# Kernel optimization log

Measured on AMD Instinct MI355X. Metric: run time of the kernel, lower is better.

The kernel has to match this reference:

```python
import jax, jax.numpy as jnp
import numpy as np

KS = 16
FREQ = jnp.array([0., 1., 2., 4., 8., 16., 32., 64.], dtype=jnp.float32)  # [0]+[2^i], d=8
TWO_PI = 2.0 * np.pi


def softplus_b10(x):
    # torch F.softplus(x, beta=10, threshold=1): linear when beta*x > threshold
    bx = 10.0 * x
    return jnp.where(bx > 1.0, x, jnp.log1p(jnp.exp(jnp.minimum(bx, 1.0))) / 10.0)


def grid_sample_2d(img, gx, gy):
    # img: (C, H, W) complex; gx,gy: (N,) in [-1,1]. Bilinear, align_corners=True,
    # zero padding -- matches torch.nn.functional.grid_sample. Returns (C, N).
    C, H, W = img.shape
    ix = (gx + 1.0) * 0.5 * (W - 1)
    iy = (gy + 1.0) * 0.5 * (H - 1)
    ix0 = jnp.floor(ix)
    iy0 = jnp.floor(iy)
    wx = ix - ix0
    wy = iy - iy0

    def corner(iyc, ixc, w):
        valid = (ixc >= 0) & (ixc <= W - 1) & (iyc >= 0) & (iyc <= H - 1)
        ii = jnp.clip(ixc, 0, W - 1).astype(jnp.int32)
        jj = jnp.clip(iyc, 0, H - 1).astype(jnp.int32)
        return img[:, jj, ii] * (w * valid)[None, :]

    return (corner(iy0, ix0, (1 - wx) * (1 - wy))
            + corner(iy0, ix0 + 1, wx * (1 - wy))
            + corner(iy0 + 1, ix0, (1 - wx) * wy)
            + corner(iy0 + 1, ix0 + 1, wx * wy))


def batch_irfft(P, x):
    # P: (ks, d, N) complex; x: (N,) in [-1,1]. Trig-weighted inverse rFFT reduce.
    xx = (x + 1.0) * 0.5
    ang = TWO_PI * xx[:, None] * FREQ[None, :]            # (N, d)
    scale = jnp.where(FREQ > 0, 2.0, 1.0)
    c = jnp.cos(ang) * scale
    s = jnp.sin(ang) * scale
    return jnp.einsum('kdn,nd->kn', P.real, c) - jnp.einsum('kdn,nd->kn', P.imag, s)


def reference(xyz, bound, alpha_params, Pu_re, Pu_im, Pv_re, Pv_im, Pw_re, Pw_im):
    alpha = softplus_b10(alpha_params)[0]
    Pu = jnp.fft.ifftn((Pu_re + 1j * Pu_im) * alpha, axes=(3, 4))  # (1,ks,dx,Ny,Nz)
    Pv = jnp.fft.ifftn((Pv_re + 1j * Pv_im) * alpha, axes=(2, 4))  # (1,ks,Nx,dy,Nz)
    Pw = jnp.fft.ifftn((Pw_re + 1j * Pw_im) * alpha, axes=(2, 3))  # (1,ks,Nx,Ny,dz)

    xyzn = xyz / bound
    xs, ys, zs = xyzn[:, 0], xyzn[:, 1], xyzn[:, 2]
    N = xs.shape[0]

    ks, dx = Pu.shape[1], Pu.shape[2]
    dy = Pv.shape[3]
    dz = Pw.shape[4]

    # Pu: sample over (Ny, Nz) plane; grid (x=zs -> width Nz, y=ys -> height Ny)
    Px = grid_sample_2d(Pu[0].reshape(ks * dx, Pu.shape[3], Pu.shape[4]), zs, ys).reshape(ks, dx, N)
    # Pv: transpose (ks,Nx,dy,Nz)->(ks,dy,Nx,Nz); grid (x=zs -> Nz, y=xs -> Nx)
    Py = grid_sample_2d(jnp.swapaxes(Pv[0], 1, 2).reshape(ks * dy, Pv.shape[2], Pv.shape[4]), zs, xs).reshape(ks, dy, N)
    # Pw: transpose (ks,Nx,Ny,dz)->(ks,dz,Ny,Nx); grid (x=xs -> Nx, y=ys -> Ny)
    Pz = grid_sample_2d(jnp.swapaxes(Pw[0], 1, 3).reshape(ks * dz, Pw.shape[3], Pw.shape[2]), xs, ys).reshape(ks, dz, N)

    P = batch_irfft(Px, xs) + batch_irfft(Py, ys) + batch_irfft(Pz, zs)  # (ks, N)
    return P.T  # (N, ks)


def setup_inputs() -> dict:
    key = jax.random.key(0)
    ks = jax.random.split(key, 8)
    N = 131072
    xyz = jax.random.uniform(ks[0], (N, 3), dtype=jnp.float32, minval=-1.0, maxval=1.0)
    scale = 0.05
    return {
        'xyz': xyz,
        'bound': 1.0,
        'alpha_params': jnp.full((1,), 0.001, dtype=jnp.float32),
        'Pu_re': scale * jax.random.normal(ks[1], (1, KS, 8, 160, 160), dtype=jnp.float32),
        'Pu_im': scale * jax.random.normal(ks[2], (1, KS, 8, 160, 160), dtype=jnp.float32),
        'Pv_re': scale * jax.random.normal(ks[3], (1, KS, 160, 8, 160), dtype=jnp.float32),
        'Pv_im': scale * jax.random.normal(ks[4], (1, KS, 160, 8, 160), dtype=jnp.float32),
        'Pw_re': scale * jax.random.normal(ks[5], (1, KS, 160, 160, 8), dtype=jnp.float32),
        'Pw_im': scale * jax.random.normal(ks[6], (1, KS, 160, 160, 8), dtype=jnp.float32),
    }
```

## Files before the change

kernel.cpp:

```cpp
#include <hip/hip_runtime.h>
#include <hip/hip_bf16.h>

#define G 160
#define GM1 159
#define KD 128
#define KP 320
#define PLANE_U 3276800
#define NBUCK 4096
#define TWO_PI_F 6.28318530717958647692f

#define TSCALE 256.0f
#define TSCALE_INV 0.00390625f

typedef __attribute__((ext_vector_type(8))) short bf16x8;
typedef __attribute__((ext_vector_type(4))) float f32x4;
typedef _Float16 half2t __attribute__((ext_vector_type(2)));
typedef __fp16 fp16x2 __attribute__((ext_vector_type(2)));

__device__ __forceinline__ unsigned short f2bf(float x) {
    unsigned u = __float_as_uint(x);
    unsigned r = (u + 0x7FFFu + ((u >> 16) & 1u)) >> 16;
    return (unsigned short)r;
}
__device__ __forceinline__ unsigned int packbf(float re, float im) {
    union { __hip_bfloat162 h; unsigned int u; } cv;
    cv.h = __float22bfloat162_rn(make_float2(re, im));
    return cv.u;
}
__device__ __forceinline__ half2t cvtpk(float a, float b) {
    union { fp16x2 f; half2t h; } cv;
    cv.f = __builtin_amdgcn_cvt_pkrtz(a, b);
    return cv.h;
}
__device__ __forceinline__ unsigned int packh(float re, float im) {
    union { fp16x2 f; unsigned int u; } cv;
    cv.f = __builtin_amdgcn_cvt_pkrtz(re, im);
    return cv.u;
}
__device__ __forceinline__ half2t u2h2(unsigned int u) {
    union { unsigned int u; half2t h; } cv;
    cv.u = u;
    return cv.h;
}
__device__ __forceinline__ float fdot2h(half2t a, half2t b, float acc) {
#if __has_builtin(__builtin_amdgcn_fdot2)
    return __builtin_amdgcn_fdot2(a, b, acc, false);
#else
    return acc + (float)a.x * (float)b.x + (float)a.y * (float)b.y;
#endif
}
__device__ __forceinline__ unsigned int wim_of(unsigned int u) {
    return ((u << 16) | (u >> 16)) ^ 0x00008000u;
}
__device__ __forceinline__ unsigned part1by2(unsigned x) {
    x &= 0x3FF;
    x = (x | (x << 16)) & 0xFF0000FFu;
    x = (x | (x << 8))  & 0x0300F00Fu;
    x = (x | (x << 4))  & 0x030C30C3u;
    x = (x | (x << 2))  & 0x09249249u;
    return x;
}
__device__ __forceinline__ unsigned morton_key(float x, float y, float z) {
    int cx = min(max((int)((x + 1.0f) * 8.0f), 0), 15);
    int cy = min(max((int)((y + 1.0f) * 8.0f), 0), 15);
    int cz = min(max((int)((z + 1.0f) * 8.0f), 0), 15);
    return part1by2(cx) | (part1by2(cy) << 1) | (part1by2(cz) << 2);
}

__global__ __launch_bounds__(256) void k_prep(
    const float* __restrict__ Pw_re, const float* __restrict__ Pw_im,
    unsigned int* __restrict__ Apw, unsigned short* __restrict__ Wre,
    unsigned int* __restrict__ counts)
{
    __shared__ unsigned int sT[64 * 33];
    int b = blockIdx.x;
    int tid = threadIdx.x;
    if (b < 16) {
        counts[b * 256 + tid] = 0;
        return;
    }
    if (b < 216) {
        int idx = (b - 16) * 256 + tid;
        int r = idx / KP, kp = idx - r * KP;
        int q = kp >> 1;
        int m = (r * q) % G;
        float th = (float)m * (TWO_PI_F / (float)G);
        float s, c;
        __sincosf(th, &s, &c);
        Wre[idx] = f2bf(((kp & 1) == 0 ? c : -s) * (1.0f / (float)G));
        return;
    }
    int b2 = b - 216;
    int k  = b2 / 100;
    int rem = b2 - k * 100;
    int pc = rem / 5;
    int q0 = (rem - pc * 5) * 32;

    int i = tid & 63, qo = tid >> 6;
    size_t base = (size_t)k * 204800 + (size_t)pc * 64 + i;
    #pragma unroll
    for (int qc = 0; qc < 8; qc++) {
        int q = q0 + qo * 8 + qc;
        float r  = Pw_re[base + (size_t)q * 1280];
        float im = Pw_im[base + (size_t)q * 1280];
        sT[i * 33 + qo * 8 + qc] = packbf(r, im);
    }
    __syncthreads();
    int qp = tid & 31, mo = tid >> 5;
    #pragma unroll
    for (int mc = 0; mc < 8; mc++) {
        int m = (k * 8 + mo) * G + pc * 8 + mc;
        Apw[(size_t)m * G + q0 + qp] = sT[(mc * 8 + mo) * 33 + qp];
    }
}

__global__ __launch_bounds__(256) void k_hist(
    const float* __restrict__ xyz, const float* __restrict__ bound,
    unsigned int* __restrict__ counts, int N)
{
    int i = blockIdx.x * blockDim.x + threadIdx.x;
    if (i >= N) return;
    float invb = 1.0f / bound[0];
    float x = xyz[3 * i + 0] * invb;
    float y = xyz[3 * i + 1] * invb;
    float z = xyz[3 * i + 2] * invb;
    atomicAdd(&counts[morton_key(x, y, z)], 1u);
}

__global__ __launch_bounds__(1024) void k_scan(
    const unsigned int* __restrict__ counts,
    unsigned int* __restrict__ cursors)
{
    __shared__ unsigned int sT[1024];
    int t = threadIdx.x;
    unsigned int local[4];
    unsigned int s = 0;
    #pragma unroll
    for (int i = 0; i < 4; i++) { local[i] = counts[t * 4 + i]; s += local[i]; }
    sT[t] = s;
    __syncthreads();
    for (int off = 1; off < 1024; off <<= 1) {
        unsigned int v = (t >= off) ? sT[t - off] : 0u;
        __syncthreads();
        sT[t] += v;
        __syncthreads();
    }
    unsigned int run = (t > 0) ? sT[t - 1] : 0u;
    #pragma unroll
    for (int i = 0; i < 4; i++) { cursors[t * 4 + i] = run; run += local[i]; }
}

__global__ __launch_bounds__(256) void k_scatter(
    const float* __restrict__ xyz, const float* __restrict__ bound,
    unsigned int* __restrict__ cursors, float4* __restrict__ sxyz, int N)
{
    int i = blockIdx.x * blockDim.x + threadIdx.x;
    if (i >= N) return;
    float invb = 1.0f / bound[0];
    float x = xyz[3 * i + 0] * invb;
    float y = xyz[3 * i + 1] * invb;
    float z = xyz[3 * i + 2] * invb;
    unsigned int pos = atomicAdd(&cursors[morton_key(x, y, z)], 1u);
    sxyz[pos] = make_float4(x, y, z, __int_as_float(i));
}

__global__ __launch_bounds__(512) void k_stage1(
    const float* __restrict__ Pu_re, const float* __restrict__ Pu_im,
    const float* __restrict__ Pv_re, const float* __restrict__ Pv_im,
    const unsigned int* __restrict__ Apw,
    const float* __restrict__ alpha_params,
    const unsigned short* __restrict__ Wre,
    unsigned int* __restrict__ Bfrag)
{
    int tid = threadIdx.x;
    int w = tid >> 6, lane = tid & 63;
    int col = lane & 15, g4 = lane >> 4;
    int gw = blockIdx.x * 8 + w;
    int mt0 = gw * 2;
    int plane = mt0 / 1280;
    int mtl0 = mt0 - plane * 1280;

    float ap = alpha_params[0];
    float bxv = 10.0f * ap;
    float alpha = (bxv > 1.0f) ? ap : log1pf(expf(fminf(bxv, 1.0f))) * 0.1f;
    alpha *= TSCALE;

    bf16x8 afr[2][10];
    #pragma unroll
    for (int ti = 0; ti < 2; ti++) {
        int mtl = mtl0 + ti;
        if (plane == 2) {
            const unsigned int* a2 = Apw + (size_t)(mtl * 16 + col) * G + g4 * 4;
            #pragma unroll
            for (int t = 0; t < 10; t++) {
                union { uint4 u; bf16x8 b; } cv;
                cv.u = *(const uint4*)(a2 + t * 16);
                afr[ti][t] = cv.b;
            }
        } else {
            const float *Ar, *Ai; int sd_, sp_;
            if (plane == 0) { Ar = Pu_re; Ai = Pu_im; sd_ = 25600; sp_ = 160; }
            else            { Ar = Pv_re; Ai = Pv_im; sd_ = 160;   sp_ = 1280; }
            int m = mtl * 16 + col;
            int k = m / 1280; int rm = m - k * 1280;
            int d = rm / 160; int p = rm - d * 160;
            size_t abase = (size_t)k * 204800 + (size_t)d * sd_ + (size_t)p * sp_ + g4 * 4;
            #pragma unroll
            for (int t = 0; t < 10; t++) {
                float4 vr = *(const float4*)(Ar + abase + t * 16);
                float4 vi = *(const float4*)(Ai + abase + t * 16);
                union { unsigned int u[4]; bf16x8 b; } cv;
                cv.u[0] = packbf(vr.x, vi.x); cv.u[1] = packbf(vr.y, vi.y);
                cv.u[2] = packbf(vr.z, vi.z); cv.u[3] = packbf(vr.w, vi.w);
                afr[ti][t] = cv.b;
            }
        }
    }

    unsigned int* Bpl = Bfrag + (size_t)plane * PLANE_U;
    int kd0 = mtl0 / 10, pt0 = mtl0 - kd0 * 10;
    int mtl1 = mtl0 + 1;
    int kd1 = mtl1 / 10, pt1 = mtl1 - kd1 * 10;

    for (int lt2 = 0; lt2 < 5; lt2++) {
        int ltA = lt2 * 2, ltB = lt2 * 2 + 1;
        f32x4 arA0 = (f32x4)(0.f), aiA0 = (f32x4)(0.f);
        f32x4 arA1 = (f32x4)(0.f), aiA1 = (f32x4)(0.f);
        f32x4 arB0 = (f32x4)(0.f), aiB0 = (f32x4)(0.f);
        f32x4 arB1 = (f32x4)(0.f), aiB1 = (f32x4)(0.f);
        const unsigned short* wpA = &Wre[(ltA * 16 + col) * KP + g4 * 8];
        const unsigned short* wpB = &Wre[(ltB * 16 + col) * KP + g4 * 8];
        #pragma unroll
        for (int t = 0; t < 10; t++) {
            union { uint4 u; bf16x8 b; } crA, ciA, crB, ciB;
            crA.u = *(const uint4*)(wpA + t * 32);
            crB.u = *(const uint4*)(wpB + t * 32);
            ciA.u.x = wim_of(crA.u.x); ciA.u.y = wim_of(crA.u.y);
            ciA.u.z = wim_of(crA.u.z); ciA.u.w = wim_of(crA.u.w);
            ciB.u.x = wim_of(crB.u.x); ciB.u.y = wim_of(crB.u.y);
            ciB.u.z = wim_of(crB.u.z); ciB.u.w = wim_of(crB.u.w);
            arA0 = __builtin_amdgcn_mfma_f32_16x16x32_bf16(afr[0][t], crA.b, arA0, 0, 0, 0);
            aiA0 = __builtin_amdgcn_mfma_f32_16x16x32_bf16(afr[0][t], ciA.b, aiA0, 0, 0, 0);
            arB0 = __builtin_amdgcn_mfma_f32_16x16x32_bf16(afr[0][t], crB.b, arB0, 0, 0, 0);
            aiB0 = __builtin_amdgcn_mfma_f32_16x16x32_bf16(afr[0][t], ciB.b, aiB0, 0, 0, 0);
            arA1 = __builtin_amdgcn_mfma_f32_16x16x32_bf16(afr[1][t], crA.b, arA1, 0, 0, 0);
            aiA1 = __builtin_amdgcn_mfma_f32_16x16x32_bf16(afr[1][t], ciA.b, aiA1, 0, 0, 0);
            arB1 = __builtin_amdgcn_mfma_f32_16x16x32_bf16(afr[1][t], crB.b, arB1, 0, 0, 0);
            aiB1 = __builtin_amdgcn_mfma_f32_16x16x32_bf16(afr[1][t], ciB.b, aiB1, 0, 0, 0);
        }
        uint4 o;
        o.x = packbf(alpha * arA0[0], alpha * aiA0[0]);
        o.y = packbf(alpha * arA0[1], alpha * aiA0[1]);
        o.z = packbf(alpha * arA0[2], alpha * aiA0[2]);
        o.w = packbf(alpha * arA0[3], alpha * aiA0[3]);
        *(uint4*)(Bpl + (size_t)(kd0 * 10 + ltA) * 2560 + pt0 * 256 + lane * 4) = o;
        o.x = packbf(alpha * arB0[0], alpha * aiB0[0]);
        o.y = packbf(alpha * arB0[1], alpha * aiB0[1]);
        o.z = packbf(alpha * arB0[2], alpha * aiB0[2]);
        o.w = packbf(alpha * arB0[3], alpha * aiB0[3]);
        *(uint4*)(Bpl + (size_t)(kd0 * 10 + ltB) * 2560 + pt0 * 256 + lane * 4) = o;
        o.x = packbf(alpha * arA1[0], alpha * aiA1[0]);
        o.y = packbf(alpha * arA1[1], alpha * aiA1[1]);
        o.z = packbf(alpha * arA1[2], alpha * aiA1[2]);
        o.w = packbf(alpha * arA1[3], alpha * aiA1[3]);
        *(uint4*)(Bpl + (size_t)(kd1 * 10 + ltA) * 2560 + pt1 * 256 + lane * 4) = o;
        o.x = packbf(alpha * arB1[0], alpha * aiB1[0]);
        o.y = packbf(alpha * arB1[1], alpha * aiB1[1]);
        o.z = packbf(alpha * arB1[2], alpha * aiB1[2]);
        o.w = packbf(alpha * arB1[3], alpha * aiB1[3]);
        *(uint4*)(Bpl + (size_t)(kd1 * 10 + ltB) * 2560 + pt1 * 256 + lane * 4) = o;
    }
}

__global__ __launch_bounds__(640) void k_stage2(
    const unsigned int* __restrict__ Bfrag,
    const unsigned short* __restrict__ Wre,
    unsigned int* __restrict__ Tall)
{
    __shared__ __align__(16) unsigned int sB[20480];
    int tid = threadIdx.x;
    int w = tid >> 6, lane = tid & 63;
    int col = lane & 15, g4 = lane >> 4;
    int kdo = blockIdx.x;
    int lt  = blockIdx.y;
    int plane = blockIdx.z;

    const unsigned int* Bp = Bfrag + (size_t)plane * PLANE_U;
    #pragma unroll
    for (int i = 0; i < 8; i++) {
        uint4 v = *(const uint4*)(Bp + ((size_t)(kdo * 8 + i) * 10 + lt) * 2560 + tid * 4);
        *(uint4*)(sB + i * 2560 + tid * 4) = v;
    }

    bf16x8 wfr[10];
    const unsigned short* wp = &Wre[(w * 16 + col) * KP + g4 * 8];
    #pragma unroll
    for (int t = 0; t < 10; t++)
        wfr[t] = *(const bf16x8*)(wp + t * 32);

    __syncthreads();

    f32x4 ar[8], ai[8];
    #pragma unroll
    for (int i = 0; i < 8; i++) { ar[i] = (f32x4)(0.f); ai[i] = (f32x4)(0.f); }

    #pragma unroll
    for (int t = 0; t < 10; t++) {
        union { bf16x8 b; uint4 u; } cr, ci;
        cr.b = wfr[t];
        ci.u.x = wim_of(cr.u.x); ci.u.y = wim_of(cr.u.y);
        ci.u.z = wim_of(cr.u.z); ci.u.w = wim_of(cr.u.w);
        #pragma unroll
        for (int kq = 0; kq < 8; kq++) {
            bf16x8 bf = *(const bf16x8*)&sB[kq * 2560 + (t * 64 + lane) * 4];
            ar[kq] = __builtin_amdgcn_mfma_f32_16x16x32_bf16(cr.b, bf, ar[kq], 0, 0, 0);
            ai[kq] = __builtin_amdgcn_mfma_f32_16x16x32_bf16(ci.b, bf, ai[kq], 0, 0, 0);
        }
    }

    unsigned int* Tp = Tall + (size_t)plane * PLANE_U;
    #pragma unroll
    for (int reg = 0; reg < 4; reg++) {
        int j = w * 16 + g4 * 4 + reg;
        int l = lt * 16 + col;
        uint4 o0, o1;
        o0.x = packh(ar[0][reg], ai[0][reg]);
        o0.y = packh(ar[1][reg], ai[1][reg]);
        o0.z = packh(ar[2][reg], ai[2][reg]);
        o0.w = packh(ar[3][reg], ai[3][reg]);
        o1.x = packh(ar[4][reg], ai[4][reg]);
        o1.y = packh(ar[5][reg], ai[5][reg]);
        o1.z = packh(ar[6][reg], ai[6][reg]);
        o1.w = packh(ar[7][reg], ai[7][reg]);
        size_t ta = ((size_t)(j * G + l)) * KD + kdo * 8;
        *(uint4*)(Tp + ta)     = o0;
        *(uint4*)(Tp + ta + 4) = o1;
    }
}

__device__ __forceinline__ void plane_addr(const unsigned int* __restrict__ T,
    float gy, float gx, int k, const unsigned int** cp, float* wv)
{
    float iy = (gy + 1.0f) * (0.5f * (float)GM1);
    float ix = (gx + 1.0f) * (0.5f * (float)GM1);
    float iy0f = floorf(iy), ix0f = floorf(ix);
    float wy = iy - iy0f, wx = ix - ix0f;
    int iy0 = (int)iy0f, ix0 = (int)ix0f;
    int iy1 = min(iy0 + 1, GM1), ix1 = min(ix0 + 1, GM1);
    iy0 = max(min(iy0, GM1), 0); ix0 = max(min(ix0, GM1), 0);
    iy1 = max(iy1, 0); ix1 = max(ix1, 0);
    cp[0] = &T[(size_t)(iy0 * G + ix0) * KD + k * 8];
    cp[1] = &T[(size_t)(iy0 * G + ix1) * KD + k * 8];
    cp[2] = &T[(size_t)(iy1 * G + ix0) * KD + k * 8];
    cp[3] = &T[(size_t)(iy1 * G + ix1) * KD + k * 8];
    wv[0] = (1.f - wx) * (1.f - wy);
    wv[1] = wx * (1.f - wy);
    wv[2] = (1.f - wx) * wy;
    wv[3] = wx * wy;
}

__device__ __forceinline__ float plane_math(const uint4* va, const uint4* vb,
                                            const float* wv, float fc)
{
    float s1v, c1v;
    __sincosf(TWO_PI_F * fc, &s1v, &c1v);
    half2t tw[8];
    tw[0] = u2h2(0x00003C00u);
    float cd = c1v, sd = s1v;
    tw[1] = cvtpk(cd + cd, -(sd + sd));
    #pragma unroll
    for (int d = 2; d < 8; d++) {
        float t2 = cd + cd;
        float cn = __builtin_fmaf(t2, cd, -1.0f);
        float sn = t2 * sd;
        cd = cn; sd = sn;
        tw[d] = cvtpk(cd + cd, -(sd + sd));
    }
    const unsigned int* a0 = (const unsigned int*)&va[0];
    const unsigned int* a1 = (const unsigned int*)&va[1];
    const unsigned int* a2 = (const unsigned int*)&va[2];
    const unsigned int* a3 = (const unsigned int*)&va[3];
    const unsigned int* b0 = (const unsigned int*)&vb[0];
    const unsigned int* b1 = (const unsigned int*)&vb[1];
    const unsigned int* b2 = (const unsigned int*)&vb[2];
    const unsigned int* b3 = (const unsigned int*)&vb[3];
    float d0 = 0.f, d1 = 0.f, d2 = 0.f, d3 = 0.f;
    #pragma unroll
    for (int d = 0; d < 4; d++) {
        half2t t = tw[d];
        d0 = fdot2h(u2h2(a0[d]), t, d0);
        d1 = fdot2h(u2h2(a1[d]), t, d1);
        d2 = fdot2h(u2h2(a2[d]), t, d2);
        d3 = fdot2h(u2h2(a3[d]), t, d3);
    }
    #pragma unroll
    for (int d = 0; d < 4; d++) {
        half2t t = tw[d + 4];
        d0 = fdot2h(u2h2(b0[d]), t, d0);
        d1 = fdot2h(u2h2(b1[d]), t, d1);
        d2 = fdot2h(u2h2(b2[d]), t, d2);
        d3 = fdot2h(u2h2(b3[d]), t, d3);
    }
    float acc = wv[0] * d0;
    acc = __builtin_fmaf(wv[1], d1, acc);
    acc = __builtin_fmaf(wv[2], d2, acc);
    acc = __builtin_fmaf(wv[3], d3, acc);
    return acc;
}

__global__ __launch_bounds__(256, 3) void k_sample(
    const float4* __restrict__ sxyz,
    const unsigned int* __restrict__ Tu, const unsigned int* __restrict__ Tv,
    const unsigned int* __restrict__ Tw,
    float* __restrict__ out, int N)
{
    int tid = threadIdx.x;
    int k = tid & 15;
    int nblocks = (N + 15) / 16;
    int seg = blockIdx.x & 7;
    int segblocks = nblocks >> 3;
    int pid = (seg * segblocks + (blockIdx.x >> 3)) * 16 + (tid >> 4);
    if (pid >= N) return;

    float4 pw = sxyz[pid];
    int n = __float_as_int(pw.w);
    float x = pw.x, y = pw.y, z = pw.z;

    const unsigned int* cp[3][4];
    float wv[3][4];
    plane_addr(Tu, y, z, k, cp[0], wv[0]);
    plane_addr(Tv, x, z, k, cp[1], wv[1]);
    plane_addr(Tw, y, x, k, cp[2], wv[2]);

    uint4 va[3][4], vb[3][4];
    #pragma unroll
    for (int pl = 0; pl < 3; pl++)
        #pragma unroll
        for (int c = 0; c < 4; c++) {
            va[pl][c] = *(const uint4*)cp[pl][c];
            vb[pl][c] = *(const uint4*)(cp[pl][c] + 4);
        }

    float acc = plane_math(va[0], vb[0], wv[0], (x + 1.0f) * 0.5f)
              + plane_math(va[1], vb[1], wv[1], (y + 1.0f) * 0.5f)
              + plane_math(va[2], vb[2], wv[2], (z + 1.0f) * 0.5f);
    out[n * 16 + k] = acc * TSCALE_INV;
}

extern "C" void kernel_launch(void* const* d_in, const int* in_sizes, int n_in,
                              void* d_out, int out_size, void* d_ws, size_t ws_size,
                              hipStream_t stream) {
    const float* xyz          = (const float*)d_in[0];
    const float* bound        = (const float*)d_in[1];
    const float* alpha_params = (const float*)d_in[2];
    const float* Pu_re = (const float*)d_in[3];
    const float* Pu_im = (const float*)d_in[4];
    const float* Pv_re = (const float*)d_in[5];
    const float* Pv_im = (const float*)d_in[6];
    const float* Pw_re = (const float*)d_in[7];
    const float* Pw_im = (const float*)d_in[8];
    float* out = (float*)d_out;
    int N = in_sizes[0] / 3;

    char* ws = (char*)d_ws;
    unsigned short* Wre  = (unsigned short*)(ws);
    unsigned int*   Apw  = (unsigned int*)(ws + 102400);
    unsigned int*   Bfr  = (unsigned int*)(ws + 102400 + 13107200);
    unsigned int*   Tall = (unsigned int*)(ws + 102400 + 13107200 + 39321600);
    char*           ws2  = ws + 102400 + 13107200 + 39321600 + 39321600;
    unsigned int*   counts  = (unsigned int*)(ws2);
    unsigned int*   cursors = (unsigned int*)(ws2 + 16384);
    float4*         sxyz    = (float4*)(ws2 + 32768);
    unsigned int*   Tu   = Tall;
    unsigned int*   Tv   = Tall + (size_t)PLANE_U;
    unsigned int*   Tw   = Tall + (size_t)2 * PLANE_U;

    k_prep<<<1816, 256, 0, stream>>>(Pw_re, Pw_im, Apw, Wre, counts);
    k_hist<<<(N + 255) / 256, 256, 0, stream>>>(xyz, bound, counts, N);
    k_scan<<<1, 1024, 0, stream>>>(counts, cursors);
    k_scatter<<<(N + 255) / 256, 256, 0, stream>>>(xyz, bound, cursors, sxyz, N);
    k_stage1<<<240, 512, 0, stream>>>(Pu_re, Pu_im, Pv_re, Pv_im, Apw,
                                      alpha_params, Wre, Bfr);
    k_stage2<<<dim3(16, 10, 3), 640, 0, stream>>>(Bfr, Wre, Tall);
    k_sample<<<(N + 15) / 16, 256, 0, stream>>>(sxyz, Tu, Tv, Tw, out, N);
}
```

Before: 262.3 us.

## Use wave-shuffle scan and halve per-wave tiles in stage1 for more blocks

```diff
diff --git a/kernel.cpp b/kernel.cpp
--- a/kernel.cpp
+++ b/kernel.cpp
@@ -131,21 +131,32 @@
     const unsigned int* __restrict__ counts,
     unsigned int* __restrict__ cursors)
 {
-    __shared__ unsigned int sT[1024];
+    __shared__ unsigned int ws[16];
     int t = threadIdx.x;
+    int lane = t & 63, wid = t >> 6;
     unsigned int local[4];
     unsigned int s = 0;
     #pragma unroll
     for (int i = 0; i < 4; i++) { local[i] = counts[t * 4 + i]; s += local[i]; }
-    sT[t] = s;
+    unsigned int sl = s;
+    #pragma unroll
+    for (int off = 1; off < 64; off <<= 1) {
+        unsigned int v = __shfl_up(s, off, 64);
+        if (lane >= off) s += v;
+    }
+    if (lane == 63) ws[wid] = s;
     __syncthreads();
-    for (int off = 1; off < 1024; off <<= 1) {
-        unsigned int v = (t >= off) ? sT[t - off] : 0u;
-        __syncthreads();
-        sT[t] += v;
-        __syncthreads();
-    }
-    unsigned int run = (t > 0) ? sT[t - 1] : 0u;
+    if (t < 16) {
+        unsigned int x = ws[t];
+        #pragma unroll
+        for (int off = 1; off < 16; off <<= 1) {
+            unsigned int v = __shfl_up(x, off, 64);
+            if (t >= off) x += v;
+        }
+        ws[t] = x;
+    }
+    __syncthreads();
+    unsigned int run = s - sl + (wid > 0 ? ws[wid - 1] : 0u);
     #pragma unroll
     for (int i = 0; i < 4; i++) { cursors[t * 4 + i] = run; run += local[i]; }
 }
@@ -164,7 +175,7 @@
     sxyz[pos] = make_float4(x, y, z, __int_as_float(i));
 }
 
-__global__ __launch_bounds__(512) void k_stage1(
+__global__ __launch_bounds__(512, 4) void k_stage1(
     const float* __restrict__ Pu_re, const float* __restrict__ Pu_im,
     const float* __restrict__ Pv_re, const float* __restrict__ Pv_im,
     const unsigned int* __restrict__ Apw,
@@ -176,58 +187,49 @@
     int w = tid >> 6, lane = tid & 63;
     int col = lane & 15, g4 = lane >> 4;
     int gw = blockIdx.x * 8 + w;
-    int mt0 = gw * 2;
-    int plane = mt0 / 1280;
-    int mtl0 = mt0 - plane * 1280;
+    int plane = gw / 1280;
+    int mtl = gw - plane * 1280;
 
     float ap = alpha_params[0];
     float bxv = 10.0f * ap;
     float alpha = (bxv > 1.0f) ? ap : log1pf(expf(fminf(bxv, 1.0f))) * 0.1f;
     alpha *= TSCALE;
 
-    bf16x8 afr[2][10];
-    #pragma unroll
-    for (int ti = 0; ti < 2; ti++) {
-        int mtl = mtl0 + ti;
-        if (plane == 2) {
-            const unsigned int* a2 = Apw + (size_t)(mtl * 16 + col) * G + g4 * 4;
-            #pragma unroll
-            for (int t = 0; t < 10; t++) {
-                union { uint4 u; bf16x8 b; } cv;
-                cv.u = *(const uint4*)(a2 + t * 16);
-                afr[ti][t] = cv.b;
-            }
-        } else {
-            const float *Ar, *Ai; int sd_, sp_;
-            if (plane == 0) { Ar = Pu_re; Ai = Pu_im; sd_ = 25600; sp_ = 160; }
-            else            { Ar = Pv_re; Ai = Pv_im; sd_ = 160;   sp_ = 1280; }
-            int m = mtl * 16 + col;
-            int k = m / 1280; int rm = m - k * 1280;
-            int d = rm / 160; int p = rm - d * 160;
-            size_t abase = (size_t)k * 204800 + (size_t)d * sd_ + (size_t)p * sp_ + g4 * 4;
-            #pragma unroll
-            for (int t = 0; t < 10; t++) {
-                float4 vr = *(const float4*)(Ar + abase + t * 16);
-                float4 vi = *(const float4*)(Ai + abase + t * 16);
-                union { unsigned int u[4]; bf16x8 b; } cv;
-                cv.u[0] = packbf(vr.x, vi.x); cv.u[1] = packbf(vr.y, vi.y);
-                cv.u[2] = packbf(vr.z, vi.z); cv.u[3] = packbf(vr.w, vi.w);
-                afr[ti][t] = cv.b;
-            }
+    bf16x8 afr[10];
+    if (plane == 2) {
+        const unsigned int* a2 = Apw + (size_t)(mtl * 16 + col) * G + g4 * 4;
+        #pragma unroll
+        for (int t = 0; t < 10; t++) {
+            union { uint4 u; bf16x8 b; } cv;
+            cv.u = *(const uint4*)(a2 + t * 16);
+            afr[t] = cv.b;
+        }
+    } else {
+        const float *Ar, *Ai; int sd_, sp_;
+        if (plane == 0) { Ar = Pu_re; Ai = Pu_im; sd_ = 25600; sp_ = 160; }
+        else            { Ar = Pv_re; Ai = Pv_im; sd_ = 160;   sp_ = 1280; }
+        int m = mtl * 16 + col;
+        int k = m / 1280; int rm = m - k * 1280;
+        int d = rm / 160; int p = rm - d * 160;
+        size_t abase = (size_t)k * 204800 + (size_t)d * sd_ + (size_t)p * sp_ + g4 * 4;
+        #pragma unroll
+        for (int t = 0; t < 10; t++) {
+            float4 vr = *(const float4*)(Ar + abase + t * 16);
+            float4 vi = *(const float4*)(Ai + abase + t * 16);
+            union { unsigned int u[4]; bf16x8 b; } cv;
+            cv.u[0] = packbf(vr.x, vi.x); cv.u[1] = packbf(vr.y, vi.y);
+            cv.u[2] = packbf(vr.z, vi.z); cv.u[3] = packbf(vr.w, vi.w);
+            afr[t] = cv.b;
         }
     }
 
     unsigned int* Bpl = Bfrag + (size_t)plane * PLANE_U;
-    int kd0 = mtl0 / 10, pt0 = mtl0 - kd0 * 10;
-    int mtl1 = mtl0 + 1;
-    int kd1 = mtl1 / 10, pt1 = mtl1 - kd1 * 10;
+    int kd = mtl / 10, pt = mtl - kd * 10;
 
     for (int lt2 = 0; lt2 < 5; lt2++) {
         int ltA = lt2 * 2, ltB = lt2 * 2 + 1;
-        f32x4 arA0 = (f32x4)(0.f), aiA0 = (f32x4)(0.f);
-        f32x4 arA1 = (f32x4)(0.f), aiA1 = (f32x4)(0.f);
-        f32x4 arB0 = (f32x4)(0.f), aiB0 = (f32x4)(0.f);
-        f32x4 arB1 = (f32x4)(0.f), aiB1 = (f32x4)(0.f);
+        f32x4 arA = (f32x4)(0.f), aiA = (f32x4)(0.f);
+        f32x4 arB = (f32x4)(0.f), aiB = (f32x4)(0.f);
         const unsigned short* wpA = &Wre[(ltA * 16 + col) * KP + g4 * 8];
         const unsigned short* wpB = &Wre[(ltB * 16 + col) * KP + g4 * 8];
         #pragma unroll
@@ -239,36 +241,22 @@
             ciA.u.z = wim_of(crA.u.z); ciA.u.w = wim_of(crA.u.w);
             ciB.u.x = wim_of(crB.u.x); ciB.u.y = wim_of(crB.u.y);
             ciB.u.z = wim_of(crB.u.z); ciB.u.w = wim_of(crB.u.w);
-            arA0 = __builtin_amdgcn_mfma_f32_16x16x32_bf16(afr[0][t], crA.b, arA0, 0, 0, 0);
-            aiA0 = __builtin_amdgcn_mfma_f32_16x16x32_bf16(afr[0][t], ciA.b, aiA0, 0, 0, 0);
-            arB0 = __builtin_amdgcn_mfma_f32_16x16x32_bf16(afr[0][t], crB.b, arB0, 0, 0, 0);
-            aiB0 = __builtin_amdgcn_mfma_f32_16x16x32_bf16(afr[0][t], ciB.b, aiB0, 0, 0, 0);
-            arA1 = __builtin_amdgcn_mfma_f32_16x16x32_bf16(afr[1][t], crA.b, arA1, 0, 0, 0);
-            aiA1 = __builtin_amdgcn_mfma_f32_16x16x32_bf16(afr[1][t], ciA.b, aiA1, 0, 0, 0);
-            arB1 = __builtin_amdgcn_mfma_f32_16x16x32_bf16(afr[1][t], crB.b, arB1, 0, 0, 0);
-            aiB1 = __builtin_amdgcn_mfma_f32_16x16x32_bf16(afr[1][t], ciB.b, aiB1, 0, 0, 0);
+            arA = __builtin_amdgcn_mfma_f32_16x16x32_bf16(afr[t], crA.b, arA, 0, 0, 0);
+            aiA = __builtin_amdgcn_mfma_f32_16x16x32_bf16(afr[t], ciA.b, aiA, 0, 0, 0);
+            arB = __builtin_amdgcn_mfma_f32_16x16x32_bf16(afr[t], crB.b, arB, 0, 0, 0);
+            aiB = __builtin_amdgcn_mfma_f32_16x16x32_bf16(afr[t], ciB.b, aiB, 0, 0, 0);
         }
         uint4 o;
-        o.x = packbf(alpha * arA0[0], alpha * aiA0[0]);
-        o.y = packbf(alpha * arA0[1], alpha * aiA0[1]);
-        o.z = packbf(alpha * arA0[2], alpha * aiA0[2]);
-        o.w = packbf(alpha * arA0[3], alpha * aiA0[3]);
-        *(uint4*)(Bpl + (size_t)(kd0 * 10 + ltA) * 2560 + pt0 * 256 + lane * 4) = o;
-        o.x = packbf(alpha * arB0[0], alpha * aiB0[0]);
-        o.y = packbf(alpha * arB0[1], alpha * aiB0[1]);
-        o.z = packbf(alpha * arB0[2], alpha * aiB0[2]);
-        o.w = packbf(alpha * arB0[3], alpha * aiB0[3]);
-        *(uint4*)(Bpl + (size_t)(kd0 * 10 + ltB) * 2560 + pt0 * 256 + lane * 4) = o;
-        o.x = packbf(alpha * arA1[0], alpha * aiA1[0]);
-        o.y = packbf(alpha * arA1[1], alpha * aiA1[1]);
-        o.z = packbf(alpha * arA1[2], alpha * aiA1[2]);
-        o.w = packbf(alpha * arA1[3], alpha * aiA1[3]);
-        *(uint4*)(Bpl + (size_t)(kd1 * 10 + ltA) * 2560 + pt1 * 256 + lane * 4) = o;
-        o.x = packbf(alpha * arB1[0], alpha * aiB1[0]);
-        o.y = packbf(alpha * arB1[1], alpha * aiB1[1]);
-        o.z = packbf(alpha * arB1[2], alpha * aiB1[2]);
-        o.w = packbf(alpha * arB1[3], alpha * aiB1[3]);
-        *(uint4*)(Bpl + (size_t)(kd1 * 10 + ltB) * 2560 + pt1 * 256 + lane * 4) = o;
+        o.x = packbf(alpha * arA[0], alpha * aiA[0]);
+        o.y = packbf(alpha * arA[1], alpha * aiA[1]);
+        o.z = packbf(alpha * arA[2], alpha * aiA[2]);
+        o.w = packbf(alpha * arA[3], alpha * aiA[3]);
+        *(uint4*)(Bpl + (size_t)(kd * 10 + ltA) * 2560 + pt * 256 + lane * 4) = o;
+        o.x = packbf(alpha * arB[0], alpha * aiB[0]);
+        o.y = packbf(alpha * arB[1], alpha * aiB[1]);
+        o.z = packbf(alpha * arB[2], alpha * aiB[2]);
+        o.w = packbf(alpha * arB[3], alpha * aiB[3]);
+        *(uint4*)(Bpl + (size_t)(kd * 10 + ltB) * 2560 + pt * 256 + lane * 4) = o;
     }
 }
 
@@ -479,7 +467,7 @@
     k_hist<<<(N + 255) / 256, 256, 0, stream>>>(xyz, bound, counts, N);
     k_scan<<<1, 1024, 0, stream>>>(counts, cursors);
     k_scatter<<<(N + 255) / 256, 256, 0, stream>>>(xyz, bound, cursors, sxyz, N);
-    k_stage1<<<240, 512, 0, stream>>>(Pu_re, Pu_im, Pv_re, Pv_im, Apw,
+    k_stage1<<<480, 512, 0, stream>>>(Pu_re, Pu_im, Pv_re, Pv_im, Apw,
                                       alpha_params, Wre, Bfr);
     k_stage2<<<dim3(16, 10, 3), 640, 0, stream>>>(Bfr, Wre, Tall);
     k_sample<<<(N + 15) / 16, 256, 0, stream>>>(sxyz, Tu, Tv, Tw, out, N);
```

Result: slower. 282.4 us (+7.7%).

## Stage DFT weights in LDS for stage1 and use wave-shuffle scan

Applied to the files above, without the earlier changes.

```diff
diff --git a/kernel.cpp b/kernel.cpp
--- a/kernel.cpp
+++ b/kernel.cpp
@@ -131,21 +131,32 @@
     const unsigned int* __restrict__ counts,
     unsigned int* __restrict__ cursors)
 {
-    __shared__ unsigned int sT[1024];
+    __shared__ unsigned int ws[16];
     int t = threadIdx.x;
+    int lane = t & 63, wid = t >> 6;
     unsigned int local[4];
     unsigned int s = 0;
     #pragma unroll
     for (int i = 0; i < 4; i++) { local[i] = counts[t * 4 + i]; s += local[i]; }
-    sT[t] = s;
+    unsigned int sl = s;
+    #pragma unroll
+    for (int off = 1; off < 64; off <<= 1) {
+        unsigned int v = __shfl_up(s, off, 64);
+        if (lane >= off) s += v;
+    }
+    if (lane == 63) ws[wid] = s;
     __syncthreads();
-    for (int off = 1; off < 1024; off <<= 1) {
-        unsigned int v = (t >= off) ? sT[t - off] : 0u;
-        __syncthreads();
-        sT[t] += v;
-        __syncthreads();
-    }
-    unsigned int run = (t > 0) ? sT[t - 1] : 0u;
+    if (t < 16) {
+        unsigned int x = ws[t];
+        #pragma unroll
+        for (int off = 1; off < 16; off <<= 1) {
+            unsigned int v = __shfl_up(x, off, 64);
+            if (t >= off) x += v;
+        }
+        ws[t] = x;
+    }
+    __syncthreads();
+    unsigned int run = s - sl + (wid > 0 ? ws[wid - 1] : 0u);
     #pragma unroll
     for (int i = 0; i < 4; i++) { cursors[t * 4 + i] = run; run += local[i]; }
 }
@@ -172,6 +183,7 @@
     const unsigned short* __restrict__ Wre,
     unsigned int* __restrict__ Bfrag)
 {
+    __shared__ __align__(16) unsigned short sW[51200];
     int tid = threadIdx.x;
     int w = tid >> 6, lane = tid & 63;
     int col = lane & 15, g4 = lane >> 4;
@@ -179,6 +191,16 @@
     int mt0 = gw * 2;
     int plane = mt0 / 1280;
     int mtl0 = mt0 - plane * 1280;
+
+    for (int chunk = tid; chunk < 6400; chunk += 512) {
+        int lt = chunk / 640;
+        int r  = chunk - lt * 640;
+        int t  = r >> 6;
+        int ln = r & 63;
+        int c  = ln & 15, g = ln >> 4;
+        uint4 v = *(const uint4*)&Wre[(lt * 16 + c) * KP + t * 32 + g * 8];
+        *(uint4*)&sW[chunk * 8] = v;
+    }
 
     float ap = alpha_params[0];
     float bxv = 10.0f * ap;
@@ -217,6 +239,8 @@
         }
     }
 
+    __syncthreads();
+
     unsigned int* Bpl = Bfrag + (size_t)plane * PLANE_U;
     int kd0 = mtl0 / 10, pt0 = mtl0 - kd0 * 10;
     int mtl1 = mtl0 + 1;
@@ -228,13 +252,13 @@
         f32x4 arA1 = (f32x4)(0.f), aiA1 = (f32x4)(0.f);
         f32x4 arB0 = (f32x4)(0.f), aiB0 = (f32x4)(0.f);
         f32x4 arB1 = (f32x4)(0.f), aiB1 = (f32x4)(0.f);
-        const unsigned short* wpA = &Wre[(ltA * 16 + col) * KP + g4 * 8];
-        const unsigned short* wpB = &Wre[(ltB * 16 + col) * KP + g4 * 8];
+        const unsigned short* wpA = &sW[(ltA * 640 + lane) * 8];
+        const unsigned short* wpB = &sW[(ltB * 640 + lane) * 8];
         #pragma unroll
         for (int t = 0; t < 10; t++) {
             union { uint4 u; bf16x8 b; } crA, ciA, crB, ciB;
-            crA.u = *(const uint4*)(wpA + t * 32);
-            crB.u = *(const uint4*)(wpB + t * 32);
+            crA.u = *(const uint4*)(wpA + t * 512);
+            crB.u = *(const uint4*)(wpB + t * 512);
             ciA.u.x = wim_of(crA.u.x); ciA.u.y = wim_of(crA.u.y);
             ciA.u.z = wim_of(crA.u.z); ciA.u.w = wim_of(crA.u.w);
             ciB.u.x = wim_of(crB.u.x); ciB.u.y = wim_of(crB.u.y);
```

New measurement: 251.4 us. -4.2%, faster.
